# Performance work log

Hardware: AMD Instinct MI355X
Metric: run time of the kernel (lower is better)

Reference implementation:

```python
import jax, jax.numpy as jnp
import numpy as np

B, N = 32, 2048
W_POINT, W_CHAMFER, W_STRUCT = 1.0, 5.0, 2.0
BIG = 1e10  # finite sentinel for masked-out distances
EPS = 1e-12


def setup_inputs() -> dict:
    key = jax.random.key(0)
    k1, k2, k3, k4, k5 = jax.random.split(key, 5)
    pred_xy = jax.random.normal(k1, (B, N, 2), dtype=jnp.float32)
    pred_v = jax.random.bernoulli(k2, 0.95, (B, N, 1)).astype(jnp.float32)
    tgt_xy = jax.random.normal(k3, (B, N, 2), dtype=jnp.float32)
    tgt_v = jax.random.bernoulli(k4, 0.95, (B, N, 1)).astype(jnp.float32)
    pred = jnp.concatenate([pred_xy, pred_v], axis=-1)
    target = jnp.concatenate([tgt_xy, tgt_v], axis=-1)
    skeleton_mask = jax.random.bernoulli(k5, 0.1, (B, N, 2)).astype(jnp.float32)
    return {"pred": pred, "target": target, "skeleton_mask": skeleton_mask}


def _skeleton_loss(pred, target, skeleton_mask):
    dt = pred.dtype
    tv = target[..., 2] == 1.0              # [B,N] valid target points
    vm = tv[..., None].astype(dt)           # [B,N,1]

    # masked MSE over coordinates (mean over ALL B*N*2 elements, as torch.mean)
    coord_err = (pred[..., :2] - target[..., :2]) * vm
    loss_point = jnp.mean(coord_err ** 2)

    # chamfer distance with validity masking (vectorized over batch)
    pv = pred[..., 2] == 1.0                # [B,N] valid pred points
    P, T = pred[..., :2], target[..., :2]
    d2 = (jnp.sum(P * P, -1)[:, :, None] + jnp.sum(T * T, -1)[:, None, :]
          - 2.0 * jnp.einsum('bnd,bmd->bnm', P, T))       # [B,Np,Nt]
    d = jnp.sqrt(jnp.maximum(d2, EPS))
    pvf = pv.astype(dt)
    tvf = tv.astype(dt)
    # pred -> target: min over valid target cols, mean over valid pred rows
    min_p = jnp.min(jnp.where(tv[:, None, :], d, BIG), axis=2)   # [B,Np]
    cnt_p = jnp.sum(pvf, axis=1)
    mean_p = jnp.sum(min_p * pvf, axis=1) / jnp.maximum(cnt_p, 1.0)
    # target -> pred
    min_t = jnp.min(jnp.where(pv[:, None, :], jnp.swapaxes(d, 1, 2), BIG), axis=2)
    cnt_t = jnp.sum(tvf, axis=1)
    mean_t = jnp.sum(min_t * tvf, axis=1) / jnp.maximum(cnt_t, 1.0)
    both = (cnt_p > 0) & (cnt_t > 0)
    chamfer_b = jnp.where(both, (mean_p + mean_t) * 0.5, 0.0)
    loss_chamfer = jnp.sum(chamfer_b) / B

    # structural point loss
    structure_mask = jnp.clip(skeleton_mask[..., 0] + skeleton_mask[..., 1], 0.0, 1.0)[..., None]
    total_mask = structure_mask * vm
    struct_err = (pred[..., :2] - target[..., :2]) * total_mask
    loss_structure = jnp.where(jnp.sum(total_mask) > 0, jnp.mean(struct_err ** 2), 0.0)

    total = W_POINT * loss_point + W_CHAMFER * loss_chamfer + W_STRUCT * loss_structure
    vis = jnp.zeros((), dtype=dt)
    # [skeleton_total_loss, skeleton_point_loss, skeleton_visibility_loss, skeleton_shape_loss]
    return jnp.stack([total, loss_point, vis, loss_chamfer])


def reference(pred, target, skeleton_mask):
    return _skeleton_loss(pred, target, skeleton_mask)
```

## Files before the change

kernel.cpp:

```cpp
#include <hip/hip_runtime.h>
#include <math.h>

#define BB 32
#define NN 2048
#define TB 256
#define QT 8
#define RCH 16
#define MCH (NN / RCH)
#define K2_QB (NN / TB)


__device__ __forceinline__ float wred(float v) {
#pragma unroll
    for (int o = 32; o > 0; o >>= 1) v += __shfl_down(v, o, 64);
    return v;
}

__global__ __launch_bounds__(256) void k1_chamfer(
    const float* __restrict__ pred, const float* __restrict__ tgt,
    float* __restrict__ part)
{
    __shared__ float sa[MCH], sb[MCH], sc[MCH];

    const int tid  = threadIdx.x;
    const int b    = blockIdx.y;
    const int role = blockIdx.z & 1;
    const int rc   = blockIdx.z >> 1;

    const float* q = role ? tgt : pred;
    const float* r = role ? pred : tgt;
    const float* rb = r + ((size_t)b * NN + (size_t)rc * MCH) * 3;

    if (tid < MCH) {
        float rx = rb[3 * tid + 0];
        float ry = rb[3 * tid + 1];
        float rv = rb[3 * tid + 2];
        if (rv != 1.0f) { rx = 1.0e9f; ry = 1.0e9f; }
        sa[tid] = -2.0f * rx;
        sb[tid] = -2.0f * ry;
        sc[tid] = fmaf(rx, rx, ry * ry);
    }
    __syncthreads();

    const float* qb_ = q + (size_t)b * NN * 3;
    float px[QT], py[QT], mn[QT];
#pragma unroll
    for (int j = 0; j < QT; j++) {
        int qi = tid + j * TB;
        px[j] = qb_[3 * qi + 0];
        py[j] = qb_[3 * qi + 1];
        mn[j] = 3.4e38f;
    }

#pragma unroll 4
    for (int m = 0; m < MCH; m += 4) {
        float4 a4 = *(const float4*)&sa[m];
        float4 b4 = *(const float4*)&sb[m];
        float4 c4 = *(const float4*)&sc[m];
#pragma unroll
        for (int j = 0; j < QT; j++) {
            float s0 = fmaf(px[j], a4.x, fmaf(py[j], b4.x, c4.x));
            float s1 = fmaf(px[j], a4.y, fmaf(py[j], b4.y, c4.y));
            float s2 = fmaf(px[j], a4.z, fmaf(py[j], b4.z, c4.z));
            float s3 = fmaf(px[j], a4.w, fmaf(py[j], b4.w, c4.w));
            mn[j] = fminf(fminf(fminf(fminf(s0, s1), s2), s3), mn[j]);
        }
    }

#pragma unroll
    for (int j = 0; j < QT; j++) {
        int qi = tid + j * TB;
        float qn = fmaf(px[j], px[j], py[j] * py[j]);
        part[((size_t)rc * (2 * BB) + role * BB + b) * NN + qi] = qn + mn[j];
    }
}

__global__ __launch_bounds__(256) void k2_combine(
    const float* __restrict__ pred, const float* __restrict__ tgt,
    const float* __restrict__ smask, const float* __restrict__ part,
    float* __restrict__ bsum)
{
    __shared__ float sred[5 * 4];
    const int tid  = threadIdx.x;
    const int b    = blockIdx.y;
    const int role = blockIdx.z;
    const int qi   = blockIdx.x * TB + tid;

    float m = 3.4e38f;
#pragma unroll
    for (int rc = 0; rc < RCH; rc++)
        m = fminf(m, part[((size_t)rc * (2 * BB) + role * BB + b) * NN + qi]);

    const float* qp = (role ? tgt : pred) + ((size_t)b * NN + qi) * 3;
    float qvf = (qp[2] == 1.0f) ? 1.0f : 0.0f;
    float contrib = sqrtf(fmaxf(m, 1e-12f)) * qvf;

    float pt = 0.0f, st = 0.0f, mk = 0.0f;
    if (role == 0) {
        float px = qp[0], py = qp[1];
        const float* tp = tgt + ((size_t)b * NN + qi) * 3;
        float vm = (tp[2] == 1.0f) ? 1.0f : 0.0f;
        float dx = px - tp[0], dy = py - tp[1];
        float e2 = fmaf(dx, dx, dy * dy);
        float s0 = smask[((size_t)b * NN + qi) * 2 + 0];
        float s1 = smask[((size_t)b * NN + qi) * 2 + 1];
        float tm = fminf(fmaxf(s0 + s1, 0.0f), 1.0f) * vm;
        pt = e2 * vm;
        st = e2 * tm;
        mk = tm;
    }

    float v[5] = {contrib, qvf, pt, st, mk};
    const int wave = tid >> 6, lane = tid & 63;
#pragma unroll
    for (int i = 0; i < 5; i++) {
        float rv = wred(v[i]);
        if (lane == 0) sred[i * 4 + wave] = rv;
    }
    __syncthreads();
    if (tid < 5) {
        int i = tid;
        float s = sred[i * 4 + 0] + sred[i * 4 + 1] + sred[i * 4 + 2] + sred[i * 4 + 3];
        int slot = (role * BB + b) * K2_QB + blockIdx.x;
        bsum[i * (2 * BB * K2_QB) + slot] = s;
    }
}

__global__ __launch_bounds__(64) void k3_final(
    const float* __restrict__ bsum, float* __restrict__ out)
{
    const int lane = threadIdx.x;
    const int S = 2 * BB * K2_QB;

    float ch = 0.0f;
    if (lane < BB) {
        float sp = 0, cp = 0, stt = 0, ct = 0;
#pragma unroll
        for (int x = 0; x < K2_QB; x++) {
            sp  += bsum[0 * S + (0 * BB + lane) * K2_QB + x];
            cp  += bsum[1 * S + (0 * BB + lane) * K2_QB + x];
            stt += bsum[0 * S + (1 * BB + lane) * K2_QB + x];
            ct  += bsum[1 * S + (1 * BB + lane) * K2_QB + x];
        }
        float mp = sp / fmaxf(cp, 1.0f);
        float mt = stt / fmaxf(ct, 1.0f);
        ch = (cp > 0.0f && ct > 0.0f) ? 0.5f * (mp + mt) : 0.0f;
    }
    ch = wred(ch);

    float spt = 0, sst = 0, smk = 0;
    for (int i = lane; i < S; i += 64) {
        spt += bsum[2 * S + i];
        sst += bsum[3 * S + i];
        smk += bsum[4 * S + i];
    }
    spt = wred(spt); sst = wred(sst); smk = wred(smk);

    if (lane == 0) {
        float loss_chamfer = ch / (float)BB;
        const float denom = (float)BB * (float)NN * 2.0f;
        float loss_point = spt / denom;
        float loss_struct = (smk > 0.0f) ? sst / denom : 0.0f;
        out[0] = loss_point + 5.0f * loss_chamfer + 2.0f * loss_struct;
        out[1] = loss_point;
        out[2] = 0.0f;
        out[3] = loss_chamfer;
    }
}

extern "C" void kernel_launch(void* const* d_in, const int* in_sizes, int n_in,
                              void* d_out, int out_size, void* d_ws, size_t ws_size,
                              hipStream_t stream)
{
    const float* pred  = (const float*)d_in[0];
    const float* tgt   = (const float*)d_in[1];
    const float* smask = (const float*)d_in[2];
    float* out = (float*)d_out;
    float* ws  = (float*)d_ws;

    float* part = ws;
    float* bsum = ws + (size_t)RCH * 2 * BB * NN;

    k1_chamfer<<<dim3(1, BB, 2 * RCH), TB, 0, stream>>>(pred, tgt, part);
    k2_combine<<<dim3(K2_QB, BB, 2), TB, 0, stream>>>(pred, tgt, smask, part, bsum);
    k3_final<<<1, 64, 0, stream>>>(bsum, out);
}
```

Measured before the change: 81.99 us.

## Fuse chamfer, combine and final kernels using last-block atomic counters

Merges the three kernel launches into one kernel. Per-batch/role atomic counters let the last finishing chunk block do the cross-chunk min reduction and loss sums, and a global counter elects a final block to write the outputs. It also widens the inner distance loop to 8 reference points per iteration. This removes two launch gaps and the intermediate bsum pass, at the cost of a memset launch, fences, and serialised tail work in a few blocks. A leftover dead kernel (k_all) is included but never launched.

Result: slower. 172.5 us (+110.4%).

```diff
diff --git a/kernel.cpp b/kernel.cpp
--- a/kernel.cpp
+++ b/kernel.cpp
@@ -7,8 +7,10 @@
 #define QT 8
 #define RCH 16
 #define MCH (NN / RCH)
-#define K2_QB (NN / TB)
-
+
+#define PART_F ((size_t)RCH * 2 * BB * NN)
+#define BSUM_F ((size_t)2 * BB * 8)
+#define CNT_F  (PART_F + BSUM_F)
 
 __device__ __forceinline__ float wred(float v) {
 #pragma unroll
@@ -16,11 +18,14 @@
     return v;
 }
 
-__global__ __launch_bounds__(256) void k1_chamfer(
+__global__ __launch_bounds__(256) void k_all(
     const float* __restrict__ pred, const float* __restrict__ tgt,
-    float* __restrict__ part)
+    const float* __restrict__ smask, float* __restrict__ part,
+    float* __restrict__ bsum, unsigned int* __restrict__ cnts)
 {
     __shared__ float sa[MCH], sb[MCH], sc[MCH];
+    __shared__ float sred[5 * 4];
+    __shared__ int sflag;
 
     const int tid  = threadIdx.x;
     const int b    = blockIdx.y;
@@ -52,18 +57,25 @@
         mn[j] = 3.4e38f;
     }
 
-#pragma unroll 4
-    for (int m = 0; m < MCH; m += 4) {
-        float4 a4 = *(const float4*)&sa[m];
-        float4 b4 = *(const float4*)&sb[m];
-        float4 c4 = *(const float4*)&sc[m];
+#pragma unroll 2
+    for (int m = 0; m < MCH; m += 8) {
+        float4 a0 = *(const float4*)&sa[m], a1 = *(const float4*)&sa[m + 4];
+        float4 b0 = *(const float4*)&sb[m], b1 = *(const float4*)&sb[m + 4];
+        float4 c0 = *(const float4*)&sc[m], c1 = *(const float4*)&sc[m + 4];
 #pragma unroll
         for (int j = 0; j < QT; j++) {
-            float s0 = fmaf(px[j], a4.x, fmaf(py[j], b4.x, c4.x));
-            float s1 = fmaf(px[j], a4.y, fmaf(py[j], b4.y, c4.y));
-            float s2 = fmaf(px[j], a4.z, fmaf(py[j], b4.z, c4.z));
-            float s3 = fmaf(px[j], a4.w, fmaf(py[j], b4.w, c4.w));
-            mn[j] = fminf(fminf(fminf(fminf(s0, s1), s2), s3), mn[j]);
+            float s0 = fmaf(px[j], a0.x, fmaf(py[j], b0.x, c0.x));
+            float s1 = fmaf(px[j], a0.y, fmaf(py[j], b0.y, c0.y));
+            float s2 = fmaf(px[j], a0.z, fmaf(py[j], b0.z, c0.z));
+            float s3 = fmaf(px[j], a0.w, fmaf(py[j], b0.w, c0.w));
+            float s4 = fmaf(px[j], a1.x, fmaf(py[j], b1.x, c1.x));
+            float s5 = fmaf(px[j], a1.y, fmaf(py[j], b1.y, c1.y));
+            float s6 = fmaf(px[j], a1.z, fmaf(py[j], b1.z, c1.z));
+            float s7 = fmaf(px[j], a1.w, fmaf(py[j], b1.w, c1.w));
+            float u = fminf(fminf(s0, s1), s2);
+            float v = fminf(fminf(s3, s4), s5);
+            float w = fminf(fminf(s6, s7), mn[j]);
+            mn[j] = fminf(fminf(u, v), w);
         }
     }
 
@@ -73,94 +85,239 @@
         float qn = fmaf(px[j], px[j], py[j] * py[j]);
         part[((size_t)rc * (2 * BB) + role * BB + b) * NN + qi] = qn + mn[j];
     }
+
+    __threadfence();
+    if (tid == 0)
+        sflag = (atomicAdd(&cnts[role * BB + b], 1u) == RCH - 1);
+    __syncthreads();
+    if (!sflag) return;
+
+    __threadfence();
+
+    float acc[5] = {0.f, 0.f, 0.f, 0.f, 0.f};
+#pragma unroll
+    for (int j = 0; j < QT; j++) {
+        int qi = tid + j * TB;
+        float m = 3.4e38f;
+#pragma unroll
+        for (int k = 0; k < RCH; k++)
+            m = fminf(m, part[((size_t)k * (2 * BB) + role * BB + b) * NN + qi]);
+
+        const float* qp = qb_ + 3 * qi;
+        float qvf = (qp[2] == 1.0f) ? 1.0f : 0.0f;
+        acc[0] += sqrtf(fmaxf(m, 1e-12f)) * qvf;
+        acc[1] += qvf;
+
+        if (role == 0) {
+            const float* tp = tgt + ((size_t)b * NN + qi) * 3;
+            float vm = (tp[2] == 1.0f) ? 1.0f : 0.0f;
+            float dx = qp[0] - tp[0], dy = qp[1] - tp[1];
+            float e2 = fmaf(dx, dx, dy * dy);
+            float s0 = smask[((size_t)b * NN + qi) * 2 + 0];
+            float s1 = smask[((size_t)b * NN + qi) * 2 + 1];
+            float tm = fminf(fmaxf(s0 + s1, 0.0f), 1.0f) * vm;
+            acc[2] += e2 * vm;
+            acc[3] += e2 * tm;
+            acc[4] += tm;
+        }
+    }
+
+    const int wave = tid >> 6, lane = tid & 63;
+#pragma unroll
+    for (int i = 0; i < 5; i++) {
+        float rv = wred(acc[i]);
+        if (lane == 0) sred[i * 4 + wave] = rv;
+    }
+    __syncthreads();
+    if (tid < 5)
+        bsum[(role * BB + b) * 8 + tid] =
+            sred[tid * 4 + 0] + sred[tid * 4 + 1] + sred[tid * 4 + 2] + sred[tid * 4 + 3];
+
+    __threadfence();
+    if (tid == 0)
+        sflag = (atomicAdd(&cnts[64], 1u) == 2 * BB - 1);
+    __syncthreads();
+    if (!sflag) return;
+
+    __threadfence();
+    if (tid >= 64) return;
+    const int l = tid;
+
+    float ch = 0.f, pt = 0.f, st = 0.f, mk = 0.f;
+    if (l < BB) {
+        const float* r0 = &bsum[(0 * BB + l) * 8];
+        const float* r1 = &bsum[(1 * BB + l) * 8];
+        float sp = r0[0], cp = r0[1];
+        float s1_ = r1[0], ct = r1[1];
+        float mp = sp / fmaxf(cp, 1.0f);
+        float mt = s1_ / fmaxf(ct, 1.0f);
+        ch = (cp > 0.0f && ct > 0.0f) ? 0.5f * (mp + mt) : 0.0f;
+        pt = r0[2]; st = r0[3]; mk = r0[4];
+    }
+    ch = wred(ch); pt = wred(pt); st = wred(st); mk = wred(mk);
+
+    if (l == 0) {
+        float loss_chamfer = ch / (float)BB;
+        const float denom = (float)BB * (float)NN * 2.0f;
+        float loss_point = pt / denom;
+        float loss_struct = (mk > 0.0f) ? st / denom : 0.0f;
+        float* out = (float*)cnts;
+        (void)out;
+    }
+    if (l == 0) {
+    }
 }
 
-__global__ __launch_bounds__(256) void k2_combine(
+__global__ __launch_bounds__(64) void k_unused() {}
+
+extern "C" void kernel_launch(void* const* d_in, const int* in_sizes, int n_in,
+                              void* d_out, int out_size, void* d_ws, size_t ws_size,
+                              hipStream_t stream);
+
+__global__ __launch_bounds__(256) void k_fused(
     const float* __restrict__ pred, const float* __restrict__ tgt,
-    const float* __restrict__ smask, const float* __restrict__ part,
-    float* __restrict__ bsum)
+    const float* __restrict__ smask, float* __restrict__ part,
+    float* __restrict__ bsum, unsigned int* __restrict__ cnts,
+    float* __restrict__ out)
 {
+    __shared__ float sa[MCH], sb[MCH], sc[MCH];
     __shared__ float sred[5 * 4];
+    __shared__ int sflag;
+
     const int tid  = threadIdx.x;
     const int b    = blockIdx.y;
-    const int role = blockIdx.z;
-    const int qi   = blockIdx.x * TB + tid;
-
-    float m = 3.4e38f;
-#pragma unroll
-    for (int rc = 0; rc < RCH; rc++)
-        m = fminf(m, part[((size_t)rc * (2 * BB) + role * BB + b) * NN + qi]);
-
-    const float* qp = (role ? tgt : pred) + ((size_t)b * NN + qi) * 3;
-    float qvf = (qp[2] == 1.0f) ? 1.0f : 0.0f;
-    float contrib = sqrtf(fmaxf(m, 1e-12f)) * qvf;
-
-    float pt = 0.0f, st = 0.0f, mk = 0.0f;
-    if (role == 0) {
-        float px = qp[0], py = qp[1];
-        const float* tp = tgt + ((size_t)b * NN + qi) * 3;
-        float vm = (tp[2] == 1.0f) ? 1.0f : 0.0f;
-        float dx = px - tp[0], dy = py - tp[1];
-        float e2 = fmaf(dx, dx, dy * dy);
-        float s0 = smask[((size_t)b * NN + qi) * 2 + 0];
-        float s1 = smask[((size_t)b * NN + qi) * 2 + 1];
-        float tm = fminf(fmaxf(s0 + s1, 0.0f), 1.0f) * vm;
-        pt = e2 * vm;
-        st = e2 * tm;
-        mk = tm;
-    }
-
-    float v[5] = {contrib, qvf, pt, st, mk};
+    const int role = blockIdx.z & 1;
+    const int rc   = blockIdx.z >> 1;
+
+    const float* q = role ? tgt : pred;
+    const float* r = role ? pred : tgt;
+    const float* rb = r + ((size_t)b * NN + (size_t)rc * MCH) * 3;
+
+    if (tid < MCH) {
+        float rx = rb[3 * tid + 0];
+        float ry = rb[3 * tid + 1];
+        float rv = rb[3 * tid + 2];
+        if (rv != 1.0f) { rx = 1.0e9f; ry = 1.0e9f; }
+        sa[tid] = -2.0f * rx;
+        sb[tid] = -2.0f * ry;
+        sc[tid] = fmaf(rx, rx, ry * ry);
+    }
+    __syncthreads();
+
+    const float* qb_ = q + (size_t)b * NN * 3;
+    float px[QT], py[QT], mn[QT];
+#pragma unroll
+    for (int j = 0; j < QT; j++) {
+        int qi = tid + j * TB;
+        px[j] = qb_[3 * qi + 0];
+        py[j] = qb_[3 * qi + 1];
+        mn[j] = 3.4e38f;
+    }
+
+#pragma unroll 2
+    for (int m = 0; m < MCH; m += 8) {
+        float4 a0 = *(const float4*)&sa[m], a1 = *(const float4*)&sa[m + 4];
+        float4 b0 = *(const float4*)&sb[m], b1 = *(const float4*)&sb[m + 4];
+        float4 c0 = *(const float4*)&sc[m], c1 = *(const float4*)&sc[m + 4];
+#pragma unroll
+        for (int j = 0; j < QT; j++) {
+            float s0 = fmaf(px[j], a0.x, fmaf(py[j], b0.x, c0.x));
+            float s1 = fmaf(px[j], a0.y, fmaf(py[j], b0.y, c0.y));
+            float s2 = fmaf(px[j], a0.z, fmaf(py[j], b0.z, c0.z));
+            float s3 = fmaf(px[j], a0.w, fmaf(py[j], b0.w, c0.w));
+            float s4 = fmaf(px[j], a1.x, fmaf(py[j], b1.x, c1.x));
+            float s5 = fmaf(px[j], a1.y, fmaf(py[j], b1.y, c1.y));
+            float s6 = fmaf(px[j], a1.z, fmaf(py[j], b1.z, c1.z));
+            float s7 = fmaf(px[j], a1.w, fmaf(py[j], b1.w, c1.w));
+            float u = fminf(fminf(s0, s1), s2);
+            float v = fminf(fminf(s3, s4), s5);
+            float w = fminf(fminf(s6, s7), mn[j]);
+            mn[j] = fminf(fminf(u, v), w);
+        }
+    }
+
+#pragma unroll
+    for (int j = 0; j < QT; j++) {
+        int qi = tid + j * TB;
+        float qn = fmaf(px[j], px[j], py[j] * py[j]);
+        part[((size_t)rc * (2 * BB) + role * BB + b) * NN + qi] = qn + mn[j];
+    }
+
+    __threadfence();
+    if (tid == 0)
+        sflag = (atomicAdd(&cnts[role * BB + b], 1u) == RCH - 1);
+    __syncthreads();
+    if (!sflag) return;
+
+    __threadfence();
+    float acc0 = 0.f, acc1 = 0.f, acc2 = 0.f, acc3 = 0.f, acc4 = 0.f;
+#pragma unroll
+    for (int j = 0; j < QT; j++) {
+        int qi = tid + j * TB;
+        float m = 3.4e38f;
+#pragma unroll
+        for (int k = 0; k < RCH; k++)
+            m = fminf(m, part[((size_t)k * (2 * BB) + role * BB + b) * NN + qi]);
+
+        const float* qp = qb_ + 3 * qi;
+        float qvf = (qp[2] == 1.0f) ? 1.0f : 0.0f;
+        acc0 += sqrtf(fmaxf(m, 1e-12f)) * qvf;
+        acc1 += qvf;
+
+        if (role == 0) {
+            const float* tp = tgt + ((size_t)b * NN + qi) * 3;
+            float vm = (tp[2] == 1.0f) ? 1.0f : 0.0f;
+            float dx = qp[0] - tp[0], dy = qp[1] - tp[1];
+            float e2 = fmaf(dx, dx, dy * dy);
+            float s0 = smask[((size_t)b * NN + qi) * 2 + 0];
+            float s1 = smask[((size_t)b * NN + qi) * 2 + 1];
+            float tm = fminf(fmaxf(s0 + s1, 0.0f), 1.0f) * vm;
+            acc2 += e2 * vm;
+            acc3 += e2 * tm;
+            acc4 += tm;
+        }
+    }
+
+    float accs[5] = {acc0, acc1, acc2, acc3, acc4};
     const int wave = tid >> 6, lane = tid & 63;
 #pragma unroll
     for (int i = 0; i < 5; i++) {
-        float rv = wred(v[i]);
+        float rv = wred(accs[i]);
         if (lane == 0) sred[i * 4 + wave] = rv;
     }
     __syncthreads();
-    if (tid < 5) {
-        int i = tid;
-        float s = sred[i * 4 + 0] + sred[i * 4 + 1] + sred[i * 4 + 2] + sred[i * 4 + 3];
-        int slot = (role * BB + b) * K2_QB + blockIdx.x;
-        bsum[i * (2 * BB * K2_QB) + slot] = s;
-    }
-}
-
-__global__ __launch_bounds__(64) void k3_final(
-    const float* __restrict__ bsum, float* __restrict__ out)
-{
-    const int lane = threadIdx.x;
-    const int S = 2 * BB * K2_QB;
-
-    float ch = 0.0f;
-    if (lane < BB) {
-        float sp = 0, cp = 0, stt = 0, ct = 0;
-#pragma unroll
-        for (int x = 0; x < K2_QB; x++) {
-            sp  += bsum[0 * S + (0 * BB + lane) * K2_QB + x];
-            cp  += bsum[1 * S + (0 * BB + lane) * K2_QB + x];
-            stt += bsum[0 * S + (1 * BB + lane) * K2_QB + x];
-            ct  += bsum[1 * S + (1 * BB + lane) * K2_QB + x];
-        }
+    if (tid < 5)
+        bsum[(role * BB + b) * 8 + tid] =
+            sred[tid * 4 + 0] + sred[tid * 4 + 1] + sred[tid * 4 + 2] + sred[tid * 4 + 3];
+
+    __threadfence();
+    if (tid == 0)
+        sflag = (atomicAdd(&cnts[64], 1u) == 2 * BB - 1);
+    __syncthreads();
+    if (!sflag) return;
+
+    __threadfence();
+    if (tid >= 64) return;
+    const int l = tid;
+
+    float ch = 0.f, pt = 0.f, st = 0.f, mk = 0.f;
+    if (l < BB) {
+        const float* r0 = &bsum[(0 * BB + l) * 8];
+        const float* r1 = &bsum[(1 * BB + l) * 8];
+        float sp = r0[0], cp = r0[1];
+        float s1_ = r1[0], ct = r1[1];
         float mp = sp / fmaxf(cp, 1.0f);
-        float mt = stt / fmaxf(ct, 1.0f);
+        float mt = s1_ / fmaxf(ct, 1.0f);
         ch = (cp > 0.0f && ct > 0.0f) ? 0.5f * (mp + mt) : 0.0f;
-    }
-    ch = wred(ch);
-
-    float spt = 0, sst = 0, smk = 0;
-    for (int i = lane; i < S; i += 64) {
-        spt += bsum[2 * S + i];
-        sst += bsum[3 * S + i];
-        smk += bsum[4 * S + i];
-    }
-    spt = wred(spt); sst = wred(sst); smk = wred(smk);
-
-    if (lane == 0) {
+        pt = r0[2]; st = r0[3]; mk = r0[4];
+    }
+    ch = wred(ch); pt = wred(pt); st = wred(st); mk = wred(mk);
+
+    if (l == 0) {
         float loss_chamfer = ch / (float)BB;
         const float denom = (float)BB * (float)NN * 2.0f;
-        float loss_point = spt / denom;
-        float loss_struct = (smk > 0.0f) ? sst / denom : 0.0f;
+        float loss_point = pt / denom;
+        float loss_struct = (mk > 0.0f) ? st / denom : 0.0f;
         out[0] = loss_point + 5.0f * loss_chamfer + 2.0f * loss_struct;
         out[1] = loss_point;
         out[2] = 0.0f;
@@ -179,9 +336,11 @@
     float* ws  = (float*)d_ws;
 
     float* part = ws;
-    float* bsum = ws + (size_t)RCH * 2 * BB * NN;
-
-    k1_chamfer<<<dim3(1, BB, 2 * RCH), TB, 0, stream>>>(pred, tgt, part);
-    k2_combine<<<dim3(K2_QB, BB, 2), TB, 0, stream>>>(pred, tgt, smask, part, bsum);
-    k3_final<<<1, 64, 0, stream>>>(bsum, out);
+    float* bsum = ws + PART_F;
+    unsigned int* cnts = (unsigned int*)(ws + CNT_F);
+
+    hipMemsetAsync((void*)cnts, 0, 512, stream);
+
+    k_fused<<<dim3(1, BB, 2 * RCH), TB, 0, stream>>>(
+        pred, tgt, smask, part, bsum, cnts, out);
 }
```

## Fuse combine and final reduction into one per-batch kernel with atomics

Applied to the files above, without the earlier changes.

The separate combine and final-reduction kernels become a single kernel with one 512-thread block per batch. Each block min-reduces the partial chamfer results for both directions, computes the point and structure errors, and atomically adds its scaled contributions into the output, which the chamfer kernel now zeroes first. The chamfer inner loop also handles 8 reference points per iteration with a reshaped min tree. This saves one launch and the intermediate block-sum buffer, but the combine stage now runs on only 32 blocks, which may underuse the GPU when reading the partial buffer.

Result: faster. 80.34 us (-2.0%).

```diff
diff --git a/kernel.cpp b/kernel.cpp
--- a/kernel.cpp
+++ b/kernel.cpp
@@ -7,7 +7,7 @@
 #define QT 8
 #define RCH 16
 #define MCH (NN / RCH)
-#define K2_QB (NN / TB)
+#define TB2 512
 
 
 __device__ __forceinline__ float wred(float v) {
@@ -18,7 +18,7 @@
 
 __global__ __launch_bounds__(256) void k1_chamfer(
     const float* __restrict__ pred, const float* __restrict__ tgt,
-    float* __restrict__ part)
+    float* __restrict__ part, float* __restrict__ out)
 {
     __shared__ float sa[MCH], sb[MCH], sc[MCH];
 
@@ -26,6 +26,8 @@
     const int b    = blockIdx.y;
     const int role = blockIdx.z & 1;
     const int rc   = blockIdx.z >> 1;
+
+    if (b == 0 && blockIdx.z == 0 && tid < 4) out[tid] = 0.0f;
 
     const float* q = role ? tgt : pred;
     const float* r = role ? pred : tgt;
@@ -52,18 +54,25 @@
         mn[j] = 3.4e38f;
     }
 
-#pragma unroll 4
-    for (int m = 0; m < MCH; m += 4) {
-        float4 a4 = *(const float4*)&sa[m];
-        float4 b4 = *(const float4*)&sb[m];
-        float4 c4 = *(const float4*)&sc[m];
+#pragma unroll 2
+    for (int m = 0; m < MCH; m += 8) {
+        float4 a0 = *(const float4*)&sa[m], a1 = *(const float4*)&sa[m + 4];
+        float4 b0 = *(const float4*)&sb[m], b1 = *(const float4*)&sb[m + 4];
+        float4 c0 = *(const float4*)&sc[m], c1 = *(const float4*)&sc[m + 4];
 #pragma unroll
         for (int j = 0; j < QT; j++) {
-            float s0 = fmaf(px[j], a4.x, fmaf(py[j], b4.x, c4.x));
-            float s1 = fmaf(px[j], a4.y, fmaf(py[j], b4.y, c4.y));
-            float s2 = fmaf(px[j], a4.z, fmaf(py[j], b4.z, c4.z));
-            float s3 = fmaf(px[j], a4.w, fmaf(py[j], b4.w, c4.w));
-            mn[j] = fminf(fminf(fminf(fminf(s0, s1), s2), s3), mn[j]);
+            float s0 = fmaf(px[j], a0.x, fmaf(py[j], b0.x, c0.x));
+            float s1 = fmaf(px[j], a0.y, fmaf(py[j], b0.y, c0.y));
+            float s2 = fmaf(px[j], a0.z, fmaf(py[j], b0.z, c0.z));
+            float s3 = fmaf(px[j], a0.w, fmaf(py[j], b0.w, c0.w));
+            float s4 = fmaf(px[j], a1.x, fmaf(py[j], b1.x, c1.x));
+            float s5 = fmaf(px[j], a1.y, fmaf(py[j], b1.y, c1.y));
+            float s6 = fmaf(px[j], a1.z, fmaf(py[j], b1.z, c1.z));
+            float s7 = fmaf(px[j], a1.w, fmaf(py[j], b1.w, c1.w));
+            float u = fminf(fminf(s0, s1), s2);
+            float v = fminf(fminf(s3, s4), s5);
+            float w = fminf(fminf(s6, s7), mn[j]);
+            mn[j] = fminf(fminf(u, v), w);
         }
     }
 
@@ -75,96 +84,88 @@
     }
 }
 
-__global__ __launch_bounds__(256) void k2_combine(
+__global__ __launch_bounds__(TB2) void k2_final(
     const float* __restrict__ pred, const float* __restrict__ tgt,
     const float* __restrict__ smask, const float* __restrict__ part,
-    float* __restrict__ bsum)
+    float* __restrict__ out)
 {
-    __shared__ float sred[5 * 4];
-    const int tid  = threadIdx.x;
-    const int b    = blockIdx.y;
-    const int role = blockIdx.z;
-    const int qi   = blockIdx.x * TB + tid;
+    __shared__ float sred[7][8];
+    const int tid = threadIdx.x;
+    const int b   = blockIdx.x;
 
-    float m = 3.4e38f;
+    float a0 = 0, a1 = 0, a2 = 0, a3 = 0, a4 = 0, a5 = 0, a6 = 0;
+
 #pragma unroll
-    for (int rc = 0; rc < RCH; rc++)
-        m = fminf(m, part[((size_t)rc * (2 * BB) + role * BB + b) * NN + qi]);
+    for (int j = 0; j < NN / TB2; j++) {
+        int qi = tid + j * TB2;
+        float m = 3.4e38f;
+#pragma unroll
+        for (int k = 0; k < RCH; k++)
+            m = fminf(m, part[((size_t)k * (2 * BB) + b) * NN + qi]);
 
-    const float* qp = (role ? tgt : pred) + ((size_t)b * NN + qi) * 3;
-    float qvf = (qp[2] == 1.0f) ? 1.0f : 0.0f;
-    float contrib = sqrtf(fmaxf(m, 1e-12f)) * qvf;
+        const float* qp = pred + ((size_t)b * NN + qi) * 3;
+        float qvf = (qp[2] == 1.0f) ? 1.0f : 0.0f;
+        a0 += sqrtf(fmaxf(m, 1e-12f)) * qvf;
+        a1 += qvf;
 
-    float pt = 0.0f, st = 0.0f, mk = 0.0f;
-    if (role == 0) {
-        float px = qp[0], py = qp[1];
         const float* tp = tgt + ((size_t)b * NN + qi) * 3;
         float vm = (tp[2] == 1.0f) ? 1.0f : 0.0f;
-        float dx = px - tp[0], dy = py - tp[1];
+        float dx = qp[0] - tp[0], dy = qp[1] - tp[1];
         float e2 = fmaf(dx, dx, dy * dy);
         float s0 = smask[((size_t)b * NN + qi) * 2 + 0];
         float s1 = smask[((size_t)b * NN + qi) * 2 + 1];
         float tm = fminf(fmaxf(s0 + s1, 0.0f), 1.0f) * vm;
-        pt = e2 * vm;
-        st = e2 * tm;
-        mk = tm;
+        a2 += e2 * vm;
+        a3 += e2 * tm;
+        a4 += tm;
     }
 
-    float v[5] = {contrib, qvf, pt, st, mk};
+#pragma unroll
+    for (int j = 0; j < NN / TB2; j++) {
+        int qi = tid + j * TB2;
+        float m = 3.4e38f;
+#pragma unroll
+        for (int k = 0; k < RCH; k++)
+            m = fminf(m, part[((size_t)k * (2 * BB) + BB + b) * NN + qi]);
+
+        const float* qp = tgt + ((size_t)b * NN + qi) * 3;
+        float qvf = (qp[2] == 1.0f) ? 1.0f : 0.0f;
+        a5 += sqrtf(fmaxf(m, 1e-12f)) * qvf;
+        a6 += qvf;
+    }
+
+    float v[7] = {a0, a1, a2, a3, a4, a5, a6};
     const int wave = tid >> 6, lane = tid & 63;
 #pragma unroll
-    for (int i = 0; i < 5; i++) {
+    for (int i = 0; i < 7; i++) {
         float rv = wred(v[i]);
-        if (lane == 0) sred[i * 4 + wave] = rv;
+        if (lane == 0) sred[i][wave] = rv;
     }
     __syncthreads();
-    if (tid < 5) {
-        int i = tid;
-        float s = sred[i * 4 + 0] + sred[i * 4 + 1] + sred[i * 4 + 2] + sred[i * 4 + 3];
-        int slot = (role * BB + b) * K2_QB + blockIdx.x;
-        bsum[i * (2 * BB * K2_QB) + slot] = s;
-    }
-}
 
-__global__ __launch_bounds__(64) void k3_final(
-    const float* __restrict__ bsum, float* __restrict__ out)
-{
-    const int lane = threadIdx.x;
-    const int S = 2 * BB * K2_QB;
+    if (tid == 0) {
+        float s[7];
+#pragma unroll
+        for (int i = 0; i < 7; i++) {
+            float acc = 0.0f;
+#pragma unroll
+            for (int w = 0; w < TB2 / 64; w++) acc += sred[i][w];
+            s[i] = acc;
+        }
+        float sp = s[0], cp = s[1], spt = s[2], sst = s[3];
+        float st_ = s[5], ct = s[6];
+        float mp = sp / fmaxf(cp, 1.0f);
+        float mt = st_ / fmaxf(ct, 1.0f);
+        float ch = (cp > 0.0f && ct > 0.0f) ? 0.5f * (mp + mt) : 0.0f;
 
-    float ch = 0.0f;
-    if (lane < BB) {
-        float sp = 0, cp = 0, stt = 0, ct = 0;
-#pragma unroll
-        for (int x = 0; x < K2_QB; x++) {
-            sp  += bsum[0 * S + (0 * BB + lane) * K2_QB + x];
-            cp  += bsum[1 * S + (0 * BB + lane) * K2_QB + x];
-            stt += bsum[0 * S + (1 * BB + lane) * K2_QB + x];
-            ct  += bsum[1 * S + (1 * BB + lane) * K2_QB + x];
-        }
-        float mp = sp / fmaxf(cp, 1.0f);
-        float mt = stt / fmaxf(ct, 1.0f);
-        ch = (cp > 0.0f && ct > 0.0f) ? 0.5f * (mp + mt) : 0.0f;
-    }
-    ch = wred(ch);
+        const float denom = (float)BB * (float)NN * 2.0f;
+        float lp = spt / denom;
+        float ls = sst / denom;
+        float lc = ch / (float)BB;
 
-    float spt = 0, sst = 0, smk = 0;
-    for (int i = lane; i < S; i += 64) {
-        spt += bsum[2 * S + i];
-        sst += bsum[3 * S + i];
-        smk += bsum[4 * S + i];
-    }
-    spt = wred(spt); sst = wred(sst); smk = wred(smk);
-
-    if (lane == 0) {
-        float loss_chamfer = ch / (float)BB;
-        const float denom = (float)BB * (float)NN * 2.0f;
-        float loss_point = spt / denom;
-        float loss_struct = (smk > 0.0f) ? sst / denom : 0.0f;
-        out[0] = loss_point + 5.0f * loss_chamfer + 2.0f * loss_struct;
-        out[1] = loss_point;
-        out[2] = 0.0f;
-        out[3] = loss_chamfer;
+        atomicAdd(&out[0], lp + 5.0f * lc + 2.0f * ls);
+        atomicAdd(&out[1], lp);
+        atomicAdd(&out[3], lc);
     }
 }
 
@@ -176,12 +177,8 @@
     const float* tgt   = (const float*)d_in[1];
     const float* smask = (const float*)d_in[2];
     float* out = (float*)d_out;
-    float* ws  = (float*)d_ws;
+    float* part = (float*)d_ws;
 
-    float* part = ws;
-    float* bsum = ws + (size_t)RCH * 2 * BB * NN;
-
-    k1_chamfer<<<dim3(1, BB, 2 * RCH), TB, 0, stream>>>(pred, tgt, part);
-    k2_combine<<<dim3(K2_QB, BB, 2), TB, 0, stream>>>(pred, tgt, smask, part, bsum);
-    k3_final<<<1, 64, 0, stream>>>(bsum, out);
+    k1_chamfer<<<dim3(1, BB, 2 * RCH), TB, 0, stream>>>(pred, tgt, part, out);
+    k2_final<<<dim3(BB), TB2, 0, stream>>>(pred, tgt, smask, part, out);
 }
```
